# Kernel tuning notes

Hardware: AMD Instinct MI355X
Metric: run time of the kernel (lower is better)

The kernel has to match this reference:

```python
import jax, jax.numpy as jnp
from jax import lax
import numpy as np

# ---- constants mirroring args ----
T = 8192          # signal length
NUM_CH = 64       # eeg channels
LSTM_SIZE = 256
NUM_CLS = 40
NUM_PROP = 1024   # candidate proposals before NMS
NUM_PROP_AFTER = 256
PROP_LEN = 128    # extracted window length
IOU_THRESH = 0.5


def setup_inputs() -> dict:
    key = jax.random.key(0)
    ks = jax.random.split(key, 12)
    data = jax.random.normal(ks[0], (T, NUM_CH), dtype=jnp.float32)
    # proposals: (start, end, score), 1-D temporal intervals
    starts = jax.random.uniform(ks[1], (NUM_PROP,), minval=0.0, maxval=float(T - PROP_LEN))
    lens = jax.random.uniform(ks[2], (NUM_PROP,), minval=32.0, maxval=float(PROP_LEN))
    scores = jax.random.uniform(ks[3], (NUM_PROP,))
    proposals = jnp.stack([starts, starts + lens, scores], axis=-1).astype(jnp.float32)

    H, C = LSTM_SIZE, NUM_CH
    s_ih = 1.0 / np.sqrt(C)
    s_hh = 1.0 / np.sqrt(H)
    W_ih = jax.random.uniform(ks[4], (4 * H, C), minval=-s_ih, maxval=s_ih)
    W_hh = jax.random.uniform(ks[5], (4 * H, H), minval=-s_hh, maxval=s_hh)
    b_ih = jax.random.uniform(ks[6], (4 * H,), minval=-s_hh, maxval=s_hh)
    b_hh = jax.random.uniform(ks[7], (4 * H,), minval=-s_hh, maxval=s_hh)
    s_h = 1.0 / np.sqrt(H)
    W_cls = jax.random.uniform(ks[8], (NUM_CLS, H), minval=-s_h, maxval=s_h)
    b_cls = jax.random.uniform(ks[9], (NUM_CLS,), minval=-s_h, maxval=s_h)
    W_bbox = jax.random.uniform(ks[10], (2 * NUM_CLS, H), minval=-s_h, maxval=s_h)
    b_bbox = jax.random.uniform(ks[11], (2 * NUM_CLS,), minval=-s_h, maxval=s_h)
    return {"data": data, "proposals": proposals, "W_ih": W_ih, "W_hh": W_hh,
            "b_ih": b_ih, "b_hh": b_hh, "W_cls": W_cls, "b_cls": b_cls,
            "W_bbox": W_bbox, "b_bbox": b_bbox}


def _nms_1d(starts, ends, scores, iou_thresh):
    """Greedy 1-D interval NMS. Returns indices (into original order) of the
    first NUM_PROP_AFTER surviving proposals, in descending-score order."""
    order = jnp.argsort(-scores)
    s, e = starts[order], ends[order]
    n = s.shape[0]
    idx = jnp.arange(n)

    def body(i, sup):
        inter = jnp.maximum(0.0, jnp.minimum(e[i], e) - jnp.maximum(s[i], s))
        union = (e[i] - s[i]) + (e - s) - inter
        iou = inter / jnp.maximum(union, 1e-6)
        new = sup | ((iou > iou_thresh) & (idx > i) & (~sup[i]))
        return new

    suppressed = lax.fori_loop(0, n, body, jnp.zeros(n, dtype=bool))
    keep = ~suppressed
    # stable sort: kept proposals first, preserving score order
    sel = jnp.argsort(jnp.where(keep, 0, 1), stable=True)[:NUM_PROP_AFTER]
    return order[sel]


def _lstm_last(x, W_ih, W_hh, b_ih, b_hh):
    """x: [K, L, C]; returns last hidden state [K, H] (torch gate order ifgo)."""
    K = x.shape[0]
    H = W_hh.shape[1]
    h0 = jnp.zeros((K, H), x.dtype)
    c0 = jnp.zeros((K, H), x.dtype)
    b = b_ih + b_hh

    def step(carry, xt):
        h, c = carry
        gates = xt @ W_ih.T + h @ W_hh.T + b  # [K, 4H]
        i, f, g, o = jnp.split(gates, 4, axis=-1)
        i = jax.nn.sigmoid(i)
        f = jax.nn.sigmoid(f)
        g = jnp.tanh(g)
        o = jax.nn.sigmoid(o)
        c = f * c + i * g
        h = o * jnp.tanh(c)
        return (h, c), None

    (h, _), _ = lax.scan(step, (h0, c0), jnp.swapaxes(x, 0, 1))
    return h


def reference(data, proposals, W_ih, W_hh, b_ih, b_hh, W_cls, b_cls, W_bbox, b_bbox):
    starts, ends, scores = proposals[:, 0], proposals[:, 1], proposals[:, 2]
    # NMS + truncate to num_prop_after (training branch of original)
    kept = _nms_1d(starts, ends, scores, IOU_THRESH)            # [K]
    # extract fixed-length eeg windows at proposal starts (gather)
    t0 = jnp.clip(jnp.round(starts[kept]).astype(jnp.int32), 0, T - PROP_LEN)
    win_idx = t0[:, None] + jnp.arange(PROP_LEN)[None, :]       # [K, L]
    eeg_proposals = data[win_idx]                               # [K, L, C]
    # region LSTM -> last timestep feature
    base_feat = _lstm_last(eeg_proposals, W_ih, W_hh, b_ih, b_hh)  # [K, H]
    cls_feat = base_feat @ W_cls.T + b_cls                      # [K, num_cls]
    bbox_feat = base_feat @ W_bbox.T + b_bbox                   # [K, 2*num_cls]
    return cls_feat, bbox_feat
```

## Files before the change

### kernel.cpp

```cpp
#include <hip/hip_runtime.h>
#include <math.h>

#define T_LEN 8192
#define NUM_CH 64
#define HID 256
#define NUM_CLS 40
#define NUM_PROP 1024
#define NUM_PROP_AFTER 256
#define PROP_LEN 128

#define MS 4
#define NGRP 64
#define NSL 4
#define KH 320
#define KSEGN 4
#define SEGH 80
#define HXPAR 65536

typedef _Float16 h2_t __attribute__((ext_vector_type(2)));
union U32H2 { unsigned int u; h2_t h; };
union HU16 { _Float16 h; unsigned short u; };

#if defined(__has_builtin)
#if __has_builtin(__builtin_amdgcn_fdot2)
#define HAS_FDOT2 1
#endif
#endif

__device__ __forceinline__ float dot2f(unsigned int wa, unsigned int hb, float acc) {
    U32H2 a, b;
    a.u = wa;
    b.u = hb;
#ifdef HAS_FDOT2
    return __builtin_amdgcn_fdot2(a.h, b.h, acc, false);
#else
    return acc + (float)a.h[0] * (float)b.h[0] + (float)a.h[1] * (float)b.h[1];
#endif
}

__device__ __forceinline__ float dot8f(const uint4& w, const uint4& h, float acc) {
    acc = dot2f(w.x, h.x, acc);
    acc = dot2f(w.y, h.y, acc);
    acc = dot2f(w.z, h.z, acc);
    acc = dot2f(w.w, h.w, acc);
    return acc;
}

__device__ __forceinline__ float fsigmoid(float x) { return 1.0f / (1.0f + __expf(-x)); }
__device__ __forceinline__ float ftanh(float x) {
    float e = __expf(-2.0f * fabsf(x));
    float t = (1.0f - e) / (1.0f + e);
    return copysignf(t, x);
}

__device__ __forceinline__ unsigned int pack2(float a, float b) {
    HU16 ha, hb;
    ha.h = (_Float16)a;
    hb.h = (_Float16)b;
    return (unsigned int)ha.u | ((unsigned int)hb.u << 16);
}

__global__ __launch_bounds__(1024, 4) void fused_kernel(
    const float* __restrict__ data, const float* __restrict__ prop,
    const float* __restrict__ W_ih, const float* __restrict__ W_hh,
    const float* __restrict__ b_ih, const float* __restrict__ b_hh,
    const float* __restrict__ W_cls, const float* __restrict__ b_cls,
    const float* __restrict__ W_bbox, const float* __restrict__ b_bbox,
    float* __restrict__ out, unsigned int* __restrict__ t0s,
    unsigned int* __restrict__ Hx32) {
    __shared__ __align__(16) _Float16 hx[MS][KH];
    __shared__ __align__(16) float pp[MS][KSEGN][256];

    const int tid = threadIdx.x;
    const int g = blockIdx.x & (NGRP - 1);
    const int s = blockIdx.x >> 6;
    const int kseg = tid >> 8;
    const int rl = tid & 255;

    if (blockIdx.x == 0) {
        float* sc_p = &pp[0][0][0];
        float* ss = &pp[1][0][0];
        float* se = &pp[2][0][0];
        unsigned char* sup = (unsigned char*)&pp[3][0][0];
        unsigned long long* cmask =
            (unsigned long long*)((char*)&pp[3][0][0] + 1024);

        float ps = prop[tid * 3 + 0];
        float pe = prop[tid * 3 + 1];
        float pc = prop[tid * 3 + 2];
        sc_p[tid] = pc;
        sup[tid] = 0;
        __syncthreads();

        int r = 0;
        for (int j = 0; j < NUM_PROP; ++j) {
            float o = sc_p[j];
            r += (o > pc) || (o == pc && j < tid);
        }
        ss[r] = ps;
        se[r] = pe;
        __syncthreads();

        const float my_s = ss[tid];
        const float my_e = se[tid];
        const float my_len = my_e - my_s;
        bool mysup = false;

        for (int ci = 0; ci < 16; ++ci) {
            if (tid < 64) {
                int i = ci * 64 + tid;
                float is_ = ss[i], ie_ = se[i];
                unsigned long long m = __ballot(sup[i] != 0);
                for (int l = 0; l < 64; ++l) {
                    if (!((m >> l) & 1)) {
                        float ls = __shfl(is_, l);
                        float le = __shfl(ie_, l);
                        float inter = fmaxf(fminf(le, ie_) - fmaxf(ls, is_), 0.0f);
                        float uni = (le - ls) + (ie_ - is_) - inter;
                        float iou = inter / fmaxf(uni, 1e-6f);
                        unsigned long long nb = __ballot((tid > l) && (iou > 0.5f));
                        m |= nb;
                    }
                }
                sup[i] = (unsigned char)((m >> tid) & 1);
                if (tid == 0) cmask[ci] = ~m;
            }
            __syncthreads();
            unsigned long long am = cmask[ci];
            for (int l = 0; l < 64; ++l) {
                if ((am >> l) & 1) {
                    int i = ci * 64 + l;
                    if (tid > i && !mysup) {
                        float ls = ss[i], le = se[i];
                        float inter = fmaxf(fminf(le, my_e) - fmaxf(ls, my_s), 0.0f);
                        float uni = (le - ls) + my_len - inter;
                        if (inter / fmaxf(uni, 1e-6f) > 0.5f) mysup = true;
                    }
                }
            }
            sup[tid] = mysup ? 1 : 0;
            __syncthreads();
        }

        int myc = tid >> 6;
        unsigned long long mybit = 1ull << (tid & 63);
        int kb = 0, kt = 0;
        for (int c2 = 0; c2 < 16; ++c2) {
            int p = __popcll(cmask[c2]);
            kt += p;
            if (c2 < myc) kb += p;
        }
        kb += __popcll(cmask[myc] & (mybit - 1));
        int slot = (cmask[myc] & mybit) ? kb : (kt + (tid - kb));
        if (slot < NUM_PROP_AFTER) {
            int t0v = (int)rintf(my_s);
            t0v = max(0, min(t0v, T_LEN - PROP_LEN));
            __hip_atomic_store(&t0s[slot], (unsigned int)t0v | 0x80000000u,
                               __ATOMIC_RELAXED, __HIP_MEMORY_SCOPE_AGENT);
        }
        asm volatile("s_waitcnt vmcnt(0)" ::: "memory");
        __syncthreads();
    }

    uint4 Wr[10];
    {
        const int gate = rl >> 6, unit = rl & 63;
        const int grow = gate * 256 + s * 64 + unit;
        const float* __restrict__ baseh = W_hh + grow * HID;
        const float* __restrict__ basex = W_ih + grow * NUM_CH;
#pragma unroll
        for (int j = 0; j < 10; ++j) {
            const int kh = kseg * SEGH + j * 8;
            const float* src = (kh < 256) ? (baseh + kh) : (basex + (kh - 256));
            float4 f0 = *(const float4*)(src);
            float4 f1 = *(const float4*)(src + 4);
            Wr[j] = make_uint4(pack2(f0.x, f0.y), pack2(f0.z, f0.w),
                               pack2(f1.x, f1.y), pack2(f1.z, f1.w));
        }
    }

    const int aq = tid >> 6;
    const int au = tid & 63;
    float bi = 0.f, bf = 0.f, bg = 0.f, bo = 0.f, c_st = 0.f;
    int xt0 = 0;
    if (tid < 256) {
        int u = s * 64 + au;
        bi = b_ih[u] + b_hh[u];
        bf = b_ih[256 + u] + b_hh[256 + u];
        bg = b_ih[512 + u] + b_hh[512 + u];
        bo = b_ih[768 + u] + b_hh[768 + u];
    }

    const int tid2 = tid - 256;
    const int gp = tid2 >> 8;
    const int gr = tid2 & 255;
    const int gsq = gr >> 6, gu = gr & 63;
    const int sp = gp + (gp >= s ? 1 : 0);
    const unsigned int* gaddr = Hx32 + (g * MS + gsq) * HID + sp * 64 + gu;

    hx[tid >> 8][tid & 255] = (_Float16)0.0f;

    if (tid < 256) {
        const unsigned int* tp = &t0s[g * MS + aq];
        unsigned int tv;
        for (;;) {
            tv = __hip_atomic_load(tp, __ATOMIC_RELAXED, __HIP_MEMORY_SCOPE_AGENT);
            if (tv & 0x80000000u) break;
            __builtin_amdgcn_s_sleep(8);
        }
        xt0 = (int)(tv & 0x7FFFFFFFu);
        hx[aq][256 + au] = (_Float16)data[xt0 * NUM_CH + au];
    }
    __syncthreads();

    for (int t = 0; t < PROP_LEN; ++t) {
        float xnext = 0.0f;
        if (tid < 256 && t + 1 < PROP_LEN)
            xnext = data[(xt0 + t + 1) * NUM_CH + au];

        float a0 = 0.f, a1 = 0.f, a2 = 0.f, a3 = 0.f;
#pragma unroll
        for (int j = 0; j < 10; ++j) {
            const int hb = kseg * SEGH + j * 8;
            uint4 h0 = *(const uint4*)&hx[0][hb];
            uint4 h1 = *(const uint4*)&hx[1][hb];
            uint4 h2 = *(const uint4*)&hx[2][hb];
            uint4 h3 = *(const uint4*)&hx[3][hb];
            uint4 w = Wr[j];
            a0 = dot8f(w, h0, a0);
            a1 = dot8f(w, h1, a1);
            a2 = dot8f(w, h2, a2);
            a3 = dot8f(w, h3, a3);
        }
        pp[0][kseg][rl] = a0;
        pp[1][kseg][rl] = a1;
        pp[2][kseg][rl] = a2;
        pp[3][kseg][rl] = a3;
        __syncthreads();

        const unsigned int tagv = (unsigned int)(t + 1);
        const int par = (t + 1) & 1;
        if (tid < 256) {
            float si = pp[aq][0][au] + pp[aq][1][au] + pp[aq][2][au] +
                       pp[aq][3][au] + bi;
            float sf = pp[aq][0][64 + au] + pp[aq][1][64 + au] +
                       pp[aq][2][64 + au] + pp[aq][3][64 + au] + bf;
            float sg = pp[aq][0][128 + au] + pp[aq][1][128 + au] +
                       pp[aq][2][128 + au] + pp[aq][3][128 + au] + bg;
            float so = pp[aq][0][192 + au] + pp[aq][1][192 + au] +
                       pp[aq][2][192 + au] + pp[aq][3][192 + au] + bo;
            float gi = fsigmoid(si), gf = fsigmoid(sf);
            float gg = ftanh(sg), go = fsigmoid(so);
            c_st = gf * c_st + gi * gg;
            float h = go * ftanh(c_st);
            HU16 hu;
            hu.h = (_Float16)h;
            __hip_atomic_store(
                &Hx32[par * HXPAR + (g * MS + aq) * HID + s * 64 + au],
                (tagv << 16) | (unsigned int)hu.u, __ATOMIC_RELAXED,
                __HIP_MEMORY_SCOPE_AGENT);
            hx[aq][s * 64 + au] = hu.h;
            if (t + 1 < PROP_LEN) hx[aq][256 + au] = (_Float16)xnext;
        } else {
            const unsigned int* ga = gaddr + par * HXPAR;
            unsigned int v =
                __hip_atomic_load(ga, __ATOMIC_RELAXED, __HIP_MEMORY_SCOPE_AGENT);
            while (__builtin_expect((v >> 16) != tagv, 0)) {
                __builtin_amdgcn_s_sleep(1);
                v = __hip_atomic_load(ga, __ATOMIC_RELAXED,
                                      __HIP_MEMORY_SCOPE_AGENT);
            }
            HU16 hv;
            hv.u = (unsigned short)(v & 0xFFFFu);
            hx[gsq][sp * 64 + gu] = hv.h;
        }
        __syncthreads();
    }

    if (tid < MS * 30) {
        int sq = tid / 30;
        int ml = tid % 30;
        int m = s * 30 + ml;
        const float* Wrow;
        float acc;
        int oidx;
        if (m < NUM_CLS) {
            Wrow = W_cls + m * HID;
            acc = b_cls[m];
            oidx = (g * MS + sq) * NUM_CLS + m;
        } else {
            int mb = m - NUM_CLS;
            Wrow = W_bbox + mb * HID;
            acc = b_bbox[mb];
            oidx = NUM_PROP_AFTER * NUM_CLS + (g * MS + sq) * 2 * NUM_CLS + mb;
        }
        const float4* w4 = (const float4*)Wrow;
        const _Float16* hp = &hx[sq][0];
        for (int c = 0; c < 32; ++c) {
            float4 wa = w4[c * 2 + 0];
            float4 wb = w4[c * 2 + 1];
            acc += (float)hp[c * 8 + 0] * wa.x + (float)hp[c * 8 + 1] * wa.y +
                   (float)hp[c * 8 + 2] * wa.z + (float)hp[c * 8 + 3] * wa.w +
                   (float)hp[c * 8 + 4] * wb.x + (float)hp[c * 8 + 5] * wb.y +
                   (float)hp[c * 8 + 6] * wb.z + (float)hp[c * 8 + 7] * wb.w;
        }
        out[oidx] = acc;
    }
}

extern "C" void kernel_launch(void* const* d_in, const int* in_sizes, int n_in,
                              void* d_out, int out_size, void* d_ws,
                              size_t ws_size, hipStream_t stream) {
    const float* data = (const float*)d_in[0];
    const float* prop = (const float*)d_in[1];
    const float* W_ih = (const float*)d_in[2];
    const float* W_hh = (const float*)d_in[3];
    const float* b_ih = (const float*)d_in[4];
    const float* b_hh = (const float*)d_in[5];
    const float* W_cls = (const float*)d_in[6];
    const float* b_cls = (const float*)d_in[7];
    const float* W_bbox = (const float*)d_in[8];
    const float* b_bbox = (const float*)d_in[9];
    float* out = (float*)d_out;

    unsigned int* t0s = (unsigned int*)d_ws;
    unsigned int* Hx32 = (unsigned int*)((char*)d_ws + 4096);

    hipMemsetAsync(d_ws, 0, 4096 + 2 * HXPAR * 4, stream);

    void* kargs[] = {(void*)&data,  (void*)&prop,   (void*)&W_ih,  (void*)&W_hh,
                     (void*)&b_ih,  (void*)&b_hh,   (void*)&W_cls, (void*)&b_cls,
                     (void*)&W_bbox, (void*)&b_bbox, (void*)&out,  (void*)&t0s,
                     (void*)&Hx32};
    hipLaunchCooperativeKernel((void*)fused_kernel, dim3(NSL * NGRP), dim3(1024),
                               kargs, 0, stream);
}
```

Before: 635.7 us.

## Ping-pong two sequence pairs per block to overlap cross-block hidden exchange with compute

Each block's four sequences are split into two groups of two that alternate half-steps. While one group computes its gate matvec and LSTM update, dedicated threads gather the other group's hidden-state slices from peer blocks through global memory. The aim is to hide the inter-block exchange latency of every recurrent step behind useful compute. The cost is twice as many block barriers per timestep and more complex tag and parity handling.

```diff
diff --git a/kernel.cpp b/kernel.cpp
--- a/kernel.cpp
+++ b/kernel.cpp
@@ -9,8 +9,7 @@
 #define NUM_PROP_AFTER 256
 #define PROP_LEN 128
 
-#define MS 4
-#define NGRP 64
+#define NPAIR 64
 #define NSL 4
 #define KH 320
 #define KSEGN 4
@@ -68,22 +67,22 @@
     const float* __restrict__ W_bbox, const float* __restrict__ b_bbox,
     float* __restrict__ out, unsigned int* __restrict__ t0s,
     unsigned int* __restrict__ Hx32) {
-    __shared__ __align__(16) _Float16 hx[MS][KH];
-    __shared__ __align__(16) float pp[MS][KSEGN][256];
+    __shared__ __align__(16) _Float16 hx[2][2][KH];
+    __shared__ __align__(16) float pp[2][2][KSEGN][256];
 
     const int tid = threadIdx.x;
-    const int g = blockIdx.x & (NGRP - 1);
+    const int p = blockIdx.x & (NPAIR - 1);
     const int s = blockIdx.x >> 6;
     const int kseg = tid >> 8;
     const int rl = tid & 255;
 
     if (blockIdx.x == 0) {
-        float* sc_p = &pp[0][0][0];
-        float* ss = &pp[1][0][0];
-        float* se = &pp[2][0][0];
-        unsigned char* sup = (unsigned char*)&pp[3][0][0];
-        unsigned long long* cmask =
-            (unsigned long long*)((char*)&pp[3][0][0] + 1024);
+        float* nb = &pp[0][0][0][0];
+        float* sc_p = nb;
+        float* ss = nb + 1024;
+        float* se = nb + 2048;
+        unsigned char* sup = (unsigned char*)(nb + 3072);
+        unsigned long long* cmask = (unsigned long long*)((char*)(nb + 3072) + 1024);
 
         float ps = prop[tid * 3 + 0];
         float pe = prop[tid * 3 + 1];
@@ -118,8 +117,8 @@
                         float inter = fmaxf(fminf(le, ie_) - fmaxf(ls, is_), 0.0f);
                         float uni = (le - ls) + (ie_ - is_) - inter;
                         float iou = inter / fmaxf(uni, 1e-6f);
-                        unsigned long long nb = __ballot((tid > l) && (iou > 0.5f));
-                        m |= nb;
+                        unsigned long long nb2 = __ballot((tid > l) && (iou > 0.5f));
+                        m |= nb2;
                     }
                 }
                 sup[i] = (unsigned char)((m >> tid) & 1);
@@ -146,9 +145,9 @@
         unsigned long long mybit = 1ull << (tid & 63);
         int kb = 0, kt = 0;
         for (int c2 = 0; c2 < 16; ++c2) {
-            int p = __popcll(cmask[c2]);
-            kt += p;
-            if (c2 < myc) kb += p;
+            int pc2 = __popcll(cmask[c2]);
+            kt += pc2;
+            if (c2 < myc) kb += pc2;
         }
         kb += __popcll(cmask[myc] & (mybit - 1));
         int slot = (cmask[myc] & mybit) ? kb : (kt + (tid - kb));
@@ -179,107 +178,144 @@
         }
     }
 
-    const int aq = tid >> 6;
-    const int au = tid & 63;
-    float bi = 0.f, bf = 0.f, bg = 0.f, bo = 0.f, c_st = 0.f;
-    int xt0 = 0;
-    if (tid < 256) {
-        int u = s * 64 + au;
+    float bi = 0.f, bf = 0.f, bg = 0.f, bo = 0.f;
+    float c_stA = 0.f, c_stB = 0.f;
+    if (tid < 128) {
+        int u = s * 64 + (tid & 63);
         bi = b_ih[u] + b_hh[u];
         bf = b_ih[256 + u] + b_hh[256 + u];
         bg = b_ih[512 + u] + b_hh[512 + u];
         bo = b_ih[768 + u] + b_hh[768 + u];
     }
 
-    const int tid2 = tid - 256;
-    const int gp = tid2 >> 8;
-    const int gr = tid2 & 255;
-    const int gsq = gr >> 6, gu = gr & 63;
-    const int sp = gp + (gp >= s ? 1 : 0);
-    const unsigned int* gaddr = Hx32 + (g * MS + gsq) * HID + sp * 64 + gu;
-
-    hx[tid >> 8][tid & 255] = (_Float16)0.0f;
-
-    if (tid < 256) {
-        const unsigned int* tp = &t0s[g * MS + aq];
+    hx[tid >> 9][(tid >> 8) & 1][tid & 255] = (_Float16)0.0f;
+
+    const int sqx = (tid >> 6) & 1;
+    const int chx = tid & 63;
+    int xt0A = 0, xt0B = 0;
+    if (tid >= 640 && tid < 768) {
         unsigned int tv;
+        const unsigned int* tpA = &t0s[4 * p + sqx];
         for (;;) {
-            tv = __hip_atomic_load(tp, __ATOMIC_RELAXED, __HIP_MEMORY_SCOPE_AGENT);
+            tv = __hip_atomic_load(tpA, __ATOMIC_RELAXED, __HIP_MEMORY_SCOPE_AGENT);
             if (tv & 0x80000000u) break;
             __builtin_amdgcn_s_sleep(8);
         }
-        xt0 = (int)(tv & 0x7FFFFFFFu);
-        hx[aq][256 + au] = (_Float16)data[xt0 * NUM_CH + au];
-    }
-    __syncthreads();
-
-    for (int t = 0; t < PROP_LEN; ++t) {
-        float xnext = 0.0f;
-        if (tid < 256 && t + 1 < PROP_LEN)
-            xnext = data[(xt0 + t + 1) * NUM_CH + au];
-
-        float a0 = 0.f, a1 = 0.f, a2 = 0.f, a3 = 0.f;
+        xt0A = (int)(tv & 0x7FFFFFFFu);
+        const unsigned int* tpB = &t0s[4 * p + 2 + sqx];
+        for (;;) {
+            tv = __hip_atomic_load(tpB, __ATOMIC_RELAXED, __HIP_MEMORY_SCOPE_AGENT);
+            if (tv & 0x80000000u) break;
+            __builtin_amdgcn_s_sleep(8);
+        }
+        xt0B = (int)(tv & 0x7FFFFFFFu);
+        hx[0][sqx][256 + chx] = (_Float16)data[xt0A * NUM_CH + chx];
+        hx[1][sqx][256 + chx] = (_Float16)data[xt0B * NUM_CH + chx];
+    }
+
+    auto gather_grp = [&](int Y, unsigned int tg) {
+        const int par = (int)(tg & 1u);
+        const int li = tid - 768;
+        const unsigned int* base = Hx32 + par * HXPAR;
+        const int sq0 = (li >= 192) ? 1 : 0;
+        const int pu0 = li - sq0 * 192;
+        const int u0 = pu0 + (pu0 >= s * 64 ? 64 : 0);
+        const unsigned int* a0p = base + (4 * p + 2 * Y + sq0) * HID + u0;
+        const bool have1 = (li < 128);
+        const int pu1 = 64 + li;
+        const int u1 = pu1 + (pu1 >= s * 64 ? 64 : 0);
+        const unsigned int* a1p = base + (4 * p + 2 * Y + 1) * HID + u1;
+        bool d0 = false, d1 = !have1;
+        for (;;) {
+            if (!d0) {
+                unsigned int v =
+                    __hip_atomic_load(a0p, __ATOMIC_RELAXED, __HIP_MEMORY_SCOPE_AGENT);
+                if ((v >> 16) == tg) {
+                    HU16 hv;
+                    hv.u = (unsigned short)(v & 0xFFFFu);
+                    hx[Y][sq0][u0] = hv.h;
+                    d0 = true;
+                }
+            }
+            if (!d1) {
+                unsigned int v =
+                    __hip_atomic_load(a1p, __ATOMIC_RELAXED, __HIP_MEMORY_SCOPE_AGENT);
+                if ((v >> 16) == tg) {
+                    HU16 hv;
+                    hv.u = (unsigned short)(v & 0xFFFFu);
+                    hx[Y][1][u1] = hv.h;
+                    d1 = true;
+                }
+            }
+            if (d0 && d1) break;
+            __builtin_amdgcn_s_sleep(1);
+        }
+    };
+
+    auto half_step = [&](int t, int X, float& CST, int XT0) {
+        float a0 = 0.f, a1 = 0.f;
 #pragma unroll
         for (int j = 0; j < 10; ++j) {
             const int hb = kseg * SEGH + j * 8;
-            uint4 h0 = *(const uint4*)&hx[0][hb];
-            uint4 h1 = *(const uint4*)&hx[1][hb];
-            uint4 h2 = *(const uint4*)&hx[2][hb];
-            uint4 h3 = *(const uint4*)&hx[3][hb];
+            uint4 h0 = *(const uint4*)&hx[X][0][hb];
+            uint4 h1 = *(const uint4*)&hx[X][1][hb];
             uint4 w = Wr[j];
             a0 = dot8f(w, h0, a0);
             a1 = dot8f(w, h1, a1);
-            a2 = dot8f(w, h2, a2);
-            a3 = dot8f(w, h3, a3);
-        }
-        pp[0][kseg][rl] = a0;
-        pp[1][kseg][rl] = a1;
-        pp[2][kseg][rl] = a2;
-        pp[3][kseg][rl] = a3;
-        __syncthreads();
-
-        const unsigned int tagv = (unsigned int)(t + 1);
-        const int par = (t + 1) & 1;
-        if (tid < 256) {
-            float si = pp[aq][0][au] + pp[aq][1][au] + pp[aq][2][au] +
-                       pp[aq][3][au] + bi;
-            float sf = pp[aq][0][64 + au] + pp[aq][1][64 + au] +
-                       pp[aq][2][64 + au] + pp[aq][3][64 + au] + bf;
-            float sg = pp[aq][0][128 + au] + pp[aq][1][128 + au] +
-                       pp[aq][2][128 + au] + pp[aq][3][128 + au] + bg;
-            float so = pp[aq][0][192 + au] + pp[aq][1][192 + au] +
-                       pp[aq][2][192 + au] + pp[aq][3][192 + au] + bo;
+        }
+        pp[X][0][kseg][rl] = a0;
+        pp[X][1][kseg][rl] = a1;
+        __syncthreads();
+
+        const unsigned int tagp = (unsigned int)(t + 1);
+        const int parp = (t + 1) & 1;
+        if (tid < 128) {
+            const int sq = tid >> 6;
+            const int au = tid & 63;
+            float si = pp[X][sq][0][au] + pp[X][sq][1][au] + pp[X][sq][2][au] +
+                       pp[X][sq][3][au] + bi;
+            float sf = pp[X][sq][0][64 + au] + pp[X][sq][1][64 + au] +
+                       pp[X][sq][2][64 + au] + pp[X][sq][3][64 + au] + bf;
+            float sg = pp[X][sq][0][128 + au] + pp[X][sq][1][128 + au] +
+                       pp[X][sq][2][128 + au] + pp[X][sq][3][128 + au] + bg;
+            float so = pp[X][sq][0][192 + au] + pp[X][sq][1][192 + au] +
+                       pp[X][sq][2][192 + au] + pp[X][sq][3][192 + au] + bo;
             float gi = fsigmoid(si), gf = fsigmoid(sf);
             float gg = ftanh(sg), go = fsigmoid(so);
-            c_st = gf * c_st + gi * gg;
-            float h = go * ftanh(c_st);
+            CST = gf * CST + gi * gg;
+            float hval = go * ftanh(CST);
             HU16 hu;
-            hu.h = (_Float16)h;
+            hu.h = (_Float16)hval;
             __hip_atomic_store(
-                &Hx32[par * HXPAR + (g * MS + aq) * HID + s * 64 + au],
-                (tagv << 16) | (unsigned int)hu.u, __ATOMIC_RELAXED,
+                &Hx32[parp * HXPAR + (4 * p + 2 * X + sq) * HID + s * 64 + au],
+                (tagp << 16) | (unsigned int)hu.u, __ATOMIC_RELAXED,
                 __HIP_MEMORY_SCOPE_AGENT);
-            hx[aq][s * 64 + au] = hu.h;
-            if (t + 1 < PROP_LEN) hx[aq][256 + au] = (_Float16)xnext;
-        } else {
-            const unsigned int* ga = gaddr + par * HXPAR;
-            unsigned int v =
-                __hip_atomic_load(ga, __ATOMIC_RELAXED, __HIP_MEMORY_SCOPE_AGENT);
-            while (__builtin_expect((v >> 16) != tagv, 0)) {
-                __builtin_amdgcn_s_sleep(1);
-                v = __hip_atomic_load(ga, __ATOMIC_RELAXED,
-                                      __HIP_MEMORY_SCOPE_AGENT);
-            }
-            HU16 hv;
-            hv.u = (unsigned short)(v & 0xFFFFu);
-            hx[gsq][sp * 64 + gu] = hv.h;
-        }
-        __syncthreads();
-    }
-
-    if (tid < MS * 30) {
-        int sq = tid / 30;
+            hx[X][sq][s * 64 + au] = hu.h;
+        } else if (tid >= 640 && tid < 768) {
+            if (t + 1 < PROP_LEN)
+                hx[X][sqx][256 + chx] = (_Float16)data[(XT0 + t + 1) * NUM_CH + chx];
+        } else if (tid >= 768) {
+            const unsigned int tg = (unsigned int)(t + X);
+            if (tg >= 1u) gather_grp(1 - X, tg);
+        }
+        __syncthreads();
+    };
+
+    __syncthreads();
+
+    for (int t = 0; t < PROP_LEN; ++t) {
+        half_step(t, 0, c_stA, xt0A);
+        half_step(t, 1, c_stB, xt0B);
+    }
+
+    if (tid >= 768) gather_grp(1, (unsigned int)PROP_LEN);
+    __syncthreads();
+
+    if (tid < 4 * 30) {
+        int sq4 = tid / 30;
         int ml = tid % 30;
+        int grp = sq4 >> 1, sq = sq4 & 1;
+        int seqg = 4 * p + 2 * grp + sq;
         int m = s * 30 + ml;
         const float* Wrow;
         float acc;
@@ -287,15 +323,15 @@
         if (m < NUM_CLS) {
             Wrow = W_cls + m * HID;
             acc = b_cls[m];
-            oidx = (g * MS + sq) * NUM_CLS + m;
+            oidx = seqg * NUM_CLS + m;
         } else {
             int mb = m - NUM_CLS;
             Wrow = W_bbox + mb * HID;
             acc = b_bbox[mb];
-            oidx = NUM_PROP_AFTER * NUM_CLS + (g * MS + sq) * 2 * NUM_CLS + mb;
+            oidx = NUM_PROP_AFTER * NUM_CLS + seqg * 2 * NUM_CLS + mb;
         }
         const float4* w4 = (const float4*)Wrow;
-        const _Float16* hp = &hx[sq][0];
+        const _Float16* hp = &hx[grp][sq][0];
         for (int c = 0; c < 32; ++c) {
             float4 wa = w4[c * 2 + 0];
             float4 wb = w4[c * 2 + 1];
@@ -332,6 +368,6 @@
                      (void*)&b_ih,  (void*)&b_hh,   (void*)&W_cls, (void*)&b_cls,
                      (void*)&W_bbox, (void*)&b_bbox, (void*)&out,  (void*)&t0s,
                      (void*)&Hx32};
-    hipLaunchCooperativeKernel((void*)fused_kernel, dim3(NSL * NGRP), dim3(1024),
+    hipLaunchCooperativeKernel((void*)fused_kernel, dim3(NSL * NPAIR), dim3(1024),
                                kargs, 0, stream);
 }
```

Result: slower. 695.2 us (+9.4%).
